# Kernel optimization log

Hardware: AMD Instinct MI355X
Metric: run time of the kernel (lower is better)

## Reference

```python
import jax, jax.numpy as jnp
import numpy as np

B, S, D, V = 4, 1024, 512, 8192
SCALES = [1, 2, 4, 8, 16]   # nn.Parameter init; used via int(scale.item()) -> static
WIN = 8                     # min(8, S//2) in compute_semantic_coherence
EPS = 1e-5


def layer_norm(x, g, b):
    m = x.mean(-1, keepdims=True)
    v = ((x - m) ** 2).mean(-1, keepdims=True)
    return (x - m) / jnp.sqrt(v + EPS) * g + b


def setup_inputs() -> dict:
    key = jax.random.key(0)
    ks = jax.random.split(key, 24)
    n = lambda k, shape, s=0.02: (jax.random.normal(k, shape, jnp.float32) * s)
    return {
        "embeddings": jax.random.normal(ks[0], (B, S, D), jnp.float32),
        "token_ids": jax.random.randint(ks[1], (B, S), 0, V),
        "context_mask": jnp.ones((B, S), jnp.float32),
        "token_similarity": n(ks[2], (V, V)),
        "W_scale": n(ks[3], (len(SCALES), D), 0.05), "b_scale": jnp.zeros((D,), jnp.float32),
        "W_sem": n(ks[4], (1, D), 0.05), "b_sem": jnp.zeros((D,), jnp.float32),
        "W_ctx": n(ks[5], (D, D), 0.02), "b_ctx": jnp.zeros((D,), jnp.float32),
        "W_fuse": n(ks[6], (4 * D, D), 0.02), "b_fuse": jnp.zeros((D,), jnp.float32),
        "ln1_g": jnp.ones((D,), jnp.float32), "ln1_b": jnp.zeros((D,), jnp.float32),
        "ln2_g": jnp.ones((D,), jnp.float32), "ln2_b": jnp.zeros((D,), jnp.float32),
        "ln3_g": jnp.ones((D,), jnp.float32), "ln3_b": jnp.zeros((D,), jnp.float32),
        "W_e0": n(ks[7], (D, D), 0.02), "b_e0": jnp.zeros((D,), jnp.float32),
        "W_e1": n(ks[8], (D, D), 0.02), "b_e1": jnp.zeros((D,), jnp.float32),
        "W_e2": n(ks[9], (D, D), 0.02), "b_e2": jnp.zeros((D,), jnp.float32),
    }


def _forward(embeddings, token_ids, context_mask, token_similarity,
             W_scale, b_scale, W_sem, b_sem, W_ctx, b_ctx, W_fuse, b_fuse,
             ln1_g, ln1_b, ln2_g, ln2_b, ln3_g, ln3_b,
             W_e0, b_e0, W_e1, b_e1, W_e2, b_e2):
    phases = jnp.tanh(embeddings)  # [B,S,D]

    # --- multi-scale coherence via cumulative sums + cos angle-difference identity ---
    # mean_t cos(p_t - m) = cos(m)*mean(cos p) + sin(m)*mean(sin p) over each window
    z = jnp.zeros((B, 1, D), phases.dtype)
    cum_p = jnp.concatenate([z, jnp.cumsum(phases, 1)], 1)            # [B,S+1,D]
    cum_c = jnp.concatenate([z, jnp.cumsum(jnp.cos(phases), 1)], 1)
    cum_s = jnp.concatenate([z, jnp.cumsum(jnp.sin(phases), 1)], 1)
    cols = []
    for s in SCALES:
        wm = (cum_p[:, s:] - cum_p[:, :-s]) / s   # window mean  [B,S-s+1,D]
        ac = (cum_c[:, s:] - cum_c[:, :-s]) / s   # window mean cos
        asn = (cum_s[:, s:] - cum_s[:, :-s]) / s  # window mean sin
        coh = jnp.mean(jnp.cos(wm) * ac + jnp.sin(wm) * asn, -1)      # [B,S-s+1]
        cols.append(jnp.pad(coh, ((0, 0), (0, s - 1))))               # torch leaves tail zeros
    msc = jnp.stack(cols, -1)                                         # [B,S,num_scales]
    scale_coh = msc @ W_scale + b_scale                               # [B,S,D]

    # --- semantic coherence (windowed, sim-weighted; torch takes mean over WHOLE tensor incl. batch) ---
    te = token_similarity[token_ids]                                  # [B,S,V]
    ten = te / jnp.maximum(jnp.linalg.norm(te, axis=-1, keepdims=True), 1e-12)
    tsim = jnp.einsum('biv,bjv->bij', ten, ten)                       # [B,S,S]
    off = jnp.arange(-WIN, WIN + 1)
    pos = jnp.arange(S)[:, None] + off[None, :]                       # [S,17]
    valid = (pos >= 0) & (pos < S)
    posc = jnp.clip(pos, 0, S - 1)
    pwin = phases[:, posc]                                            # [B,S,17,D]
    swin = jnp.take_along_axis(tsim, jnp.broadcast_to(posc[None], (B, S, 2 * WIN + 1)), axis=2)
    coh = jnp.cos((phases[:, :, None, :] - pwin) * swin[..., None]) * valid[None, :, :, None].astype(phases.dtype)
    counts = valid.sum(1).astype(phases.dtype)                        # [S]
    sem = coh.sum((0, 2, 3)) / (B * counts * D)                       # [S] (same scalar for all batches)
    sem = jnp.broadcast_to(sem[None, :], (B, S))[..., None]           # [B,S,1]
    sem_coh = sem @ W_sem + b_sem                                     # [B,S,D]

    # --- context coherence (context_mask path) ---
    cmean = jnp.mean(embeddings * context_mask[..., None], 1, keepdims=True)
    ctx_coh = jnp.cos(embeddings - cmean) @ W_ctx + b_ctx

    # --- local coherence ---
    lc = jnp.cos(embeddings[:, 1:] - embeddings[:, :-1])
    lc = jnp.concatenate([lc, jnp.zeros((B, 1, D), embeddings.dtype)], 1)

    allc = jnp.concatenate([scale_coh, sem_coh, ctx_coh, lc], -1)     # [B,S,4D]
    x = layer_norm(allc @ W_fuse + b_fuse, ln1_g, ln1_b)
    x = jax.nn.gelu(x, approximate=False)                             # dropout = identity (eval)
    for W, bb in ((W_e0, b_e0), (W_e1, b_e1), (W_e2, b_e2)):
        r = x
        h = layer_norm(x, ln2_g, ln2_b) @ W + bb
        x = r + jax.nn.gelu(h, approximate=False) * 0.1
    return layer_norm(x, ln3_g, ln3_b)


def reference(embeddings, token_ids, context_mask, token_similarity,
              W_scale, b_scale, W_sem, b_sem, W_ctx, b_ctx, W_fuse, b_fuse,
              ln1_g, ln1_b, ln2_g, ln2_b, ln3_g, ln3_b,
              W_e0, b_e0, W_e1, b_e1, W_e2, b_e2):
    return _forward(embeddings, token_ids, context_mask, token_similarity,
                    W_scale, b_scale, W_sem, b_sem, W_ctx, b_ctx, W_fuse, b_fuse,
                    ln1_g, ln1_b, ln2_g, ln2_b, ln3_g, ln3_b,
                    W_e0, b_e0, W_e1, b_e1, W_e2, b_e2)
```

## Files before the change

### kernel.cpp

```cpp
#include <hip/hip_runtime.h>


#define DEV __device__ __forceinline__
typedef unsigned short u16;
typedef __bf16 bf16x8 __attribute__((ext_vector_type(8)));
typedef float f32x4 __attribute__((ext_vector_type(4)));

static constexpr int S = 1024;
static constexpr int D = 512;
static constexpr int KCAT = 1056;

DEV u16 f2bf(float f) {
  unsigned u = __float_as_uint(f);
  return (u16)((u + 0x7fffu + ((u >> 16) & 1u)) >> 16);
}
DEV float gelu(float x) { return 0.5f * x * (1.f + erff(x * 0.70710678118654752f)); }
DEV float wred(float v) {
#pragma unroll
  for (int off = 32; off; off >>= 1) v += __shfl_down(v, off, 64);
  return v;
}
DEV void bred2(float& a, float& b, float* sm, int tid) {
  a = wred(a); b = wred(b);
  int w = tid >> 6;
  if ((tid & 63) == 0) { sm[w] = a; sm[w + 4] = b; }
  __syncthreads();
  a = sm[0] + sm[1] + sm[2] + sm[3];
  b = sm[4] + sm[5] + sm[6] + sm[7];
  __syncthreads();
}
DEV float qred(float v) {
  v += __shfl_xor(v, 1, 64);
  v += __shfl_xor(v, 2, 64);
  return v;
}

__global__ __launch_bounds__(256) void k_pre(const float* __restrict__ emb,
                                             const float* __restrict__ mask,
                                             float* __restrict__ ph,
                                             float* __restrict__ cmacc) {
  int blk = blockIdx.x, tid = threadIdx.x;
  if (blk < 1024) {
    int idx = blk * 256 + tid;
#pragma unroll
    for (int r = 0; r < 2; ++r, idx += 262144) {
      float4 v = ((const float4*)emb)[idx];
      float4 o;
      o.x = tanhf(v.x); o.y = tanhf(v.y); o.z = tanhf(v.z); o.w = tanhf(v.w);
      ((float4*)ph)[idx] = o;
    }
  } else {
    int r = blk - 1024, b = r >> 3, chunk = r & 7;
    float a0 = 0.f, a1 = 0.f;
    for (int s = chunk * 128; s < chunk * 128 + 128; ++s) {
      float m = mask[b * S + s];
      const float* row = emb + (size_t)(b * S + s) * D;
      a0 += row[tid] * m; a1 += row[tid + 256] * m;
    }
    atomicAdd(cmacc + b * D + tid, a0);
    atomicAdd(cmacc + b * D + tid + 256, a1);
  }
}

static constexpr int CP = 129;
__global__ __launch_bounds__(256) void k_dots(const float* __restrict__ sim,
                                              const int* __restrict__ tok,
                                              float* __restrict__ dots_raw,
                                              float* __restrict__ normsq) {
  __shared__ float sT[72 * CP];
  __shared__ int stok[72];
  int bx = blockIdx.x, cy = blockIdx.y, tid = threadIdx.x;
  int b = bx >> 4, g0 = (bx & 15) * 64, gidx = b * S + g0;
  if (tid < 72) {
    int p = g0 + tid;
    stok[tid] = (p < S) ? tok[b * S + p] : -1;
  }
  __syncthreads();
  const float4* sim4 = (const float4*)sim;
#pragma unroll
  for (int it = 0; it < 9; ++it) {
    int u = it * 256 + tid, r = u >> 5, q = u & 31;
    int tk = stok[r];
    float4 v = make_float4(0.f, 0.f, 0.f, 0.f);
    if (tk >= 0) v = sim4[(size_t)tk * 2048 + cy * 32 + q];
    float* dst = &sT[r * CP + 4 * q];
    dst[0] = v.x; dst[1] = v.y; dst[2] = v.z; dst[3] = v.w;
  }
  __syncthreads();
  int wave = tid >> 6, lane = tid & 63;
  float acc[9] = {};
  const float* base = &sT[lane * CP + wave * 32];
#pragma unroll 4
  for (int cc = 0; cc < 32; ++cc) {
    float va = base[cc];
    acc[8] += va * va;
#pragma unroll
    for (int o = 1; o <= 8; ++o) acc[o - 1] += va * base[o * CP + cc];
  }
  __syncthreads();
  float* red = sT;
#pragma unroll
  for (int s = 0; s < 9; ++s) red[(wave * 9 + s) * 64 + lane] = acc[s];
  __syncthreads();
  for (int u = tid; u < 576; u += 256) {
    int s = u >> 6, a = u & 63;
    float v = red[s * 64 + a] + red[(9 + s) * 64 + a] +
              red[(18 + s) * 64 + a] + red[(27 + s) * 64 + a];
    if (s < 8) atomicAdd(&dots_raw[(size_t)(gidx + a) * 8 + s], v);
    else       atomicAdd(&normsq[gidx + a], v);
  }
}

static constexpr int CP2 = 132;
__global__ __launch_bounds__(256) void k_coh(const float* __restrict__ ph,
                                             const float* __restrict__ dots_raw,
                                             const float* __restrict__ normsq,
                                             float* __restrict__ msc_raw,
                                             float* __restrict__ semacc) {
  __shared__ float sP[88 * CP2];
  __shared__ float sw2[64 * 17];
  int bx = blockIdx.x, dy = blockIdx.y, tid = threadIdx.x;
  int b = bx >> 4, g0 = (bx & 15) * 64;
  const float4* ph4 = (const float4*)ph;
#pragma unroll
  for (int it = 0; it < 11; ++it) {
    int u = it * 256 + tid, r = u >> 5, q = u & 31;
    int gr = g0 - 8 + r;
    gr = gr < 0 ? 0 : (gr > S - 1 ? S - 1 : gr);
    float4 v = ph4[(size_t)(b * S + gr) * 128 + dy * 32 + q];
    *(float4*)&sP[r * CP2 + 4 * q] = v;
  }
  for (int u = tid; u < 1088; u += 256) {
    int a = u / 17, oi = u - a * 17;
    int i = g0 + a, o = oi - 8, j = i + o;
    int idx = b * S + i;
    float v = 0.f;
    if (j >= 0 && j < S) {
      if (o == 0) v = 1.f;
      else {
        float dr = (o > 0) ? dots_raw[(size_t)idx * 8 + o - 1]
                           : dots_raw[(size_t)(idx + o) * 8 + (-o - 1)];
        float ni = fmaxf(sqrtf(normsq[idx]), 1e-12f);
        float nj = fmaxf(sqrtf(normsq[idx + o]), 1e-12f);
        v = dr / (ni * nj);
      }
    }
    sw2[u] = v;
  }
  __syncthreads();
  int ar = tid >> 2, dq = tid & 3;
  int i = g0 + ar, idx = b * S + i;
  int jmax = S - 1 - i; if (jmax > 15) jmax = 15;
  float swr[17];
#pragma unroll
  for (int oi = 0; oi < 17; ++oi) swr[oi] = sw2[ar * 17 + oi];
  float a0 = 0.f, a1 = 0.f, a2 = 0.f, a3 = 0.f, a4 = 0.f, asem = 0.f;
#pragma unroll 2
  for (int dd = 0; dd < 32; ++dd) {
    int d = dq + 4 * dd;
    const float* pb = &sP[(ar + 8) * CP2 + d];
    float sp = 0.f, sc = 0.f, ss = 0.f;
#pragma unroll
    for (int j = 0; j < 16; ++j) {
      float x = (j <= jmax) ? pb[j * CP2] : 0.f;
      sp += x; sc += __cosf(x); ss += __sinf(x);
      if (j == 0) a0 += __cosf(sp) * sc + __sinf(sp) * ss;
      else if (j == 1)  { float wm = sp * 0.5f;    a1 += __cosf(wm) * (sc * 0.5f)    + __sinf(wm) * (ss * 0.5f); }
      else if (j == 3)  { float wm = sp * 0.25f;   a2 += __cosf(wm) * (sc * 0.25f)   + __sinf(wm) * (ss * 0.25f); }
      else if (j == 7)  { float wm = sp * 0.125f;  a3 += __cosf(wm) * (sc * 0.125f)  + __sinf(wm) * (ss * 0.125f); }
      else if (j == 15) { float wm = sp * 0.0625f; a4 += __cosf(wm) * (sc * 0.0625f) + __sinf(wm) * (ss * 0.0625f); }
    }
    float p0 = pb[0];
    const float* qb = &sP[ar * CP2 + d];
#pragma unroll
    for (int oi = 0; oi < 17; ++oi) {
      int j = i + oi - 8;
      bool valid = (j >= 0) && (j < S);
      float pj = qb[oi * CP2];
      asem += valid ? __cosf((p0 - pj) * swr[oi]) : 0.f;
    }
  }
  a0 = qred(a0); a1 = qred(a1); a2 = qred(a2); a3 = qred(a3); a4 = qred(a4);
  asem = qred(asem);
  if (dq == 0) {
    float* mr = msc_raw + (size_t)idx * 5;
    atomicAdd(mr + 0, a0); atomicAdd(mr + 1, a1); atomicAdd(mr + 2, a2);
    atomicAdd(mr + 3, a3); atomicAdd(mr + 4, a4);
    atomicAdd(semacc + i, asem);
  }
}

__global__ __launch_bounds__(256) void k_wbig(const float* __restrict__ W0,
    const float* __restrict__ W1, const float* __restrict__ W2,
    const float* __restrict__ Wf, const float* __restrict__ wctx,
    const float* __restrict__ Wsc, const float* __restrict__ Wsm,
    const float* __restrict__ bsc, const float* __restrict__ bsm,
    const float* __restrict__ bcx,
    u16* __restrict__ T0, u16* __restrict__ T1, u16* __restrict__ T2,
    u16* __restrict__ wcatT, float* __restrict__ ctx_acc,
    float* __restrict__ sm_acc) {
  __shared__ float tile[64][65];
  int blk = blockIdx.x, tid = threadIdx.x;
  if (blk < 256) {
    int z = blk >> 6, rem = blk & 63;
    const float* src = z == 0 ? W0 : z == 1 ? W1 : z == 2 ? W2 : Wf + (size_t)1536 * 512;
    int r0 = (rem >> 3) * 64, c0 = (rem & 7) * 64;
    int tr = tid >> 6, tc = tid & 63;
#pragma unroll 4
    for (int i = 0; i < 16; ++i)
      tile[tr + i * 4][tc] = src[(size_t)(r0 + tr + i * 4) * 512 + c0 + tc];
    __syncthreads();
#pragma unroll 4
    for (int i = 0; i < 16; ++i) {
      int n = c0 + tr + i * 4, k = r0 + tc;
      u16 v = f2bf(tile[tc][tr + i * 4]);
      if (z == 3) wcatT[(size_t)n * KCAT + 512 + k] = v;
      else (z == 0 ? T0 : z == 1 ? T1 : T2)[(size_t)n * 512 + k] = v;
    }
  } else if (blk < 512) {
    int rem = blk - 256;
    int n = (rem & 1) * 256 + tid;
    int kbase = ((rem & 63) >> 1) * 16;
    int j0 = (rem >> 6) * 128;
    float acc[16] = {};
    for (int j = j0; j < j0 + 128; ++j) {
      float wf3 = Wf[(size_t)(1024 + j) * 512 + n];
#pragma unroll
      for (int kk = 0; kk < 16; ++kk) acc[kk] += wctx[(size_t)(kbase + kk) * 512 + j] * wf3;
    }
#pragma unroll
    for (int kk = 0; kk < 16; ++kk)
      atomicAdd(&ctx_acc[(size_t)(kbase + kk) * 512 + n], acc[kk]);
  } else {
    int rem = blk - 512;
    int n = (rem & 1) * 256 + tid;
    int j0 = (rem >> 1) * 16;
    float a0 = 0.f, a1 = 0.f, a2 = 0.f, a3 = 0.f, a4 = 0.f, au = 0.f, ac = 0.f;
    for (int j = j0; j < j0 + 16; ++j) {
      float wf1 = Wf[(size_t)j * 512 + n];
      float wf2 = Wf[(size_t)(512 + j) * 512 + n];
      float wf3 = Wf[(size_t)(1024 + j) * 512 + n];
      a0 += Wsc[j] * wf1; a1 += Wsc[512 + j] * wf1; a2 += Wsc[1024 + j] * wf1;
      a3 += Wsc[1536 + j] * wf1; a4 += Wsc[2048 + j] * wf1;
      au += Wsm[j] * wf2;
      ac += bsc[j] * wf1 + bsm[j] * wf2 + bcx[j] * wf3;
    }
    atomicAdd(&sm_acc[0 * 512 + n], a0);
    atomicAdd(&sm_acc[1 * 512 + n], a1);
    atomicAdd(&sm_acc[2 * 512 + n], a2);
    atomicAdd(&sm_acc[3 * 512 + n], a3);
    atomicAdd(&sm_acc[4 * 512 + n], a4);
    atomicAdd(&sm_acc[5 * 512 + n], au);
    atomicAdd(&sm_acc[6 * 512 + n], ac);
  }
}

__global__ __launch_bounds__(256) void k_packfin(const float* __restrict__ ctx_acc,
    const float* __restrict__ sm_acc, const float* __restrict__ bfu,
    u16* __restrict__ wcatT) {
  __shared__ float tile[64][65];
  int blk = blockIdx.x, tid = threadIdx.x;
  if (blk < 64) {
    int r0 = (blk >> 3) * 64, c0 = (blk & 7) * 64;
    int tr = tid >> 6, tc = tid & 63;
#pragma unroll 4
    for (int i = 0; i < 16; ++i)
      tile[tr + i * 4][tc] = ctx_acc[(size_t)(r0 + tr + i * 4) * 512 + c0 + tc];
    __syncthreads();
#pragma unroll 4
    for (int i = 0; i < 16; ++i)
      wcatT[(size_t)(c0 + tr + i * 4) * KCAT + r0 + tc] = f2bf(tile[tc][tr + i * 4]);
  } else {
    int n = (blk - 64) * 256 + tid;
    u16* row = wcatT + (size_t)n * KCAT;
#pragma unroll
    for (int s = 0; s < 6; ++s) row[1024 + s] = f2bf(sm_acc[s * 512 + n]);
    row[1030] = f2bf(sm_acc[6 * 512 + n] + bfu[n]);
    for (int k = 1031; k < KCAT; ++k) row[k] = 0;
  }
}

__global__ __launch_bounds__(256) void k_xcat(const float* __restrict__ emb,
    const float* __restrict__ cmacc, const float* __restrict__ msc_raw,
    const float* __restrict__ semacc, u16* __restrict__ xcat) {
  int idx = blockIdx.x, b = idx >> 10, i = idx & 1023, tid = threadIdx.x;
  const float* erow = emb + (size_t)idx * D;
  u16* orow = xcat + (size_t)idx * KCAT;
  for (int c = tid; c < KCAT; c += 256) {
    float v;
    if (c < 512) {
      v = __cosf(erow[c] - cmacc[b * D + c] * (1.f / 1024.f));
    } else if (c < 1024) {
      int d = c - 512;
      v = (i < S - 1) ? __cosf(erow[D + d] - erow[d]) : 0.f;
    } else if (c < 1029) {
      int s = c - 1024, req = (1 << s) - 1;
      v = (S - 1 - i >= req) ? msc_raw[(size_t)idx * 5 + s] * (1.f / 512.f) : 0.f;
    } else if (c == 1029) {
      int cnt = ((i < 8) ? i : 8) + ((S - 1 - i < 8) ? (S - 1 - i) : 8) + 1;
      v = semacc[i] / (4.f * (float)cnt * 512.f);
    } else if (c == 1030) {
      v = 1.f;
    } else v = 0.f;
    orow[c] = f2bf(v);
  }
}

__global__ __launch_bounds__(256) void k_gemm(const u16* __restrict__ A,
    const u16* __restrict__ BT, float* __restrict__ C,
    const float* __restrict__ bias, int K) {
  __shared__ __align__(16) u16 sA[64 * 40];
  __shared__ __align__(16) u16 sB[64 * 40];
  int tid = threadIdx.x, wave = tid >> 6, lane = tid & 63;
  int m0 = blockIdx.x * 64, n0 = blockIdx.y * 64;
  int lr = tid >> 2, lc = (tid & 3) * 8;
  int q8 = (lane >> 4) * 8, l15 = lane & 15;
  const u16* Ap = A + (size_t)(m0 + lr) * K + lc;
  const u16* Bp = BT + (size_t)(n0 + lr) * K + lc;
  f32x4 acc[4] = {};
  for (int k0 = 0; k0 < K; k0 += 32) {
    *(uint4*)&sA[lr * 40 + lc] = *(const uint4*)(Ap + k0);
    *(uint4*)&sB[lr * 40 + lc] = *(const uint4*)(Bp + k0);
    __syncthreads();
    bf16x8 af = *(const bf16x8*)&sA[(wave * 16 + l15) * 40 + q8];
#pragma unroll
    for (int f = 0; f < 4; ++f) {
      bf16x8 bfr = *(const bf16x8*)&sB[(f * 16 + l15) * 40 + q8];
      acc[f] = __builtin_amdgcn_mfma_f32_16x16x32_bf16(af, bfr, acc[f], 0, 0, 0);
    }
    __syncthreads();
  }
  int r0 = m0 + wave * 16 + (lane >> 4) * 4;
#pragma unroll
  for (int f = 0; f < 4; ++f) {
    int col = n0 + f * 16 + l15;
    float bv = bias ? bias[col] : 0.f;
#pragma unroll
    for (int r = 0; r < 4; ++r)
      C[(size_t)(r0 + r) * 512 + col] = acc[f][r] + bv;
  }
}

__global__ __launch_bounds__(256) void k_post_y1(const float* __restrict__ y,
    float* __restrict__ x, u16* __restrict__ t,
    const float* __restrict__ g1, const float* __restrict__ b1,
    const float* __restrict__ g2, const float* __restrict__ b2) {
  __shared__ float sm[8];
  int row = blockIdx.x, tid = threadIdx.x;
  size_t base = (size_t)row * 512;
  float v0 = y[base + tid], v1 = y[base + tid + 256];
  float s = v0 + v1, ss = v0 * v0 + v1 * v1;
  bred2(s, ss, sm, tid);
  float m = s * (1.f / 512.f);
  float inv = rsqrtf(ss * (1.f / 512.f) - m * m + 1e-5f);
  float x0 = gelu((v0 - m) * inv * g1[tid] + b1[tid]);
  float x1 = gelu((v1 - m) * inv * g1[tid + 256] + b1[tid + 256]);
  x[base + tid] = x0; x[base + tid + 256] = x1;
  s = x0 + x1; ss = x0 * x0 + x1 * x1;
  bred2(s, ss, sm, tid);
  m = s * (1.f / 512.f);
  inv = rsqrtf(ss * (1.f / 512.f) - m * m + 1e-5f);
  t[base + tid] = f2bf((x0 - m) * inv * g2[tid] + b2[tid]);
  t[base + tid + 256] = f2bf((x1 - m) * inv * g2[tid + 256] + b2[tid + 256]);
}

__global__ __launch_bounds__(256) void k_post_res(const float* __restrict__ h,
    float* __restrict__ x, u16* __restrict__ t, float* __restrict__ out,
    const float* __restrict__ g, const float* __restrict__ bb, int final_) {
  __shared__ float sm[8];
  int row = blockIdx.x, tid = threadIdx.x;
  size_t base = (size_t)row * 512;
  float x0 = x[base + tid] + 0.1f * gelu(h[base + tid]);
  float x1 = x[base + tid + 256] + 0.1f * gelu(h[base + tid + 256]);
  float s = x0 + x1, ss = x0 * x0 + x1 * x1;
  bred2(s, ss, sm, tid);
  float m = s * (1.f / 512.f);
  float inv = rsqrtf(ss * (1.f / 512.f) - m * m + 1e-5f);
  float n0 = (x0 - m) * inv * g[tid] + bb[tid];
  float n1 = (x1 - m) * inv * g[tid + 256] + bb[tid + 256];
  if (final_) {
    out[base + tid] = n0; out[base + tid + 256] = n1;
  } else {
    x[base + tid] = x0; x[base + tid + 256] = x1;
    t[base + tid] = f2bf(n0); t[base + tid + 256] = f2bf(n1);
  }
}

extern "C" void kernel_launch(void* const* d_in, const int* in_sizes, int n_in,
                              void* d_out, int out_size, void* d_ws, size_t ws_size,
                              hipStream_t stream) {
  const float* emb     = (const float*)d_in[0];
  const int*   tok     = (const int*)d_in[1];
  const float* mask    = (const float*)d_in[2];
  const float* sim     = (const float*)d_in[3];
  const float* W_scale = (const float*)d_in[4];
  const float* b_scale = (const float*)d_in[5];
  const float* W_sem   = (const float*)d_in[6];
  const float* b_sem   = (const float*)d_in[7];
  const float* W_ctx   = (const float*)d_in[8];
  const float* b_ctx   = (const float*)d_in[9];
  const float* W_fuse  = (const float*)d_in[10];
  const float* b_fuse  = (const float*)d_in[11];
  const float* ln1_g = (const float*)d_in[12], *ln1_b = (const float*)d_in[13];
  const float* ln2_g = (const float*)d_in[14], *ln2_b = (const float*)d_in[15];
  const float* ln3_g = (const float*)d_in[16], *ln3_b = (const float*)d_in[17];
  const float* W_e0 = (const float*)d_in[18], *b_e0 = (const float*)d_in[19];
  const float* W_e1 = (const float*)d_in[20], *b_e1 = (const float*)d_in[21];
  const float* W_e2 = (const float*)d_in[22], *b_e2 = (const float*)d_in[23];
  float* out = (float*)d_out;

  char* w = (char*)d_ws; size_t off = 0;
  auto alloc = [&](size_t bytes) { void* p = w + off; off += (bytes + 255) & ~(size_t)255; return p; };
  float* phases = (float*)alloc((size_t)4096 * 512 * 4);
  float* hbuf   = (float*)alloc((size_t)4096 * 512 * 4);
  float* xbuf   = (float*)alloc((size_t)4096 * 512 * 4);
  u16*   tbuf   = (u16*)  alloc((size_t)4096 * 512 * 2);
  u16*   xcat   = (u16*)  alloc((size_t)4096 * KCAT * 2);
  u16*   wcatT  = (u16*)  alloc((size_t)512 * KCAT * 2);
  u16*   We0T   = (u16*)  alloc((size_t)512 * 512 * 2);
  u16*   We1T   = (u16*)  alloc((size_t)512 * 512 * 2);
  u16*   We2T   = (u16*)  alloc((size_t)512 * 512 * 2);
  float* semacc   = (float*)alloc((size_t)1024 * 4);
  float* cmacc    = (float*)alloc((size_t)4 * 512 * 4);
  float* dots_raw = (float*)alloc((size_t)4096 * 8 * 4);
  float* normsq   = (float*)alloc((size_t)4096 * 4);
  float* msc_raw  = (float*)alloc((size_t)4096 * 5 * 4);
  float* ctx_acc  = (float*)alloc((size_t)512 * 512 * 4);
  float* sm_acc   = (float*)alloc((size_t)7 * 512 * 4);
  (void)ws_size; (void)in_sizes; (void)n_in; (void)out_size;

  size_t zbytes = (size_t)(1024 + 4 * 512 + 4096 * 8 + 4096 + 4096 * 5 + 512 * 512 + 7 * 512) * 4;
  hipMemsetAsync(semacc, 0, zbytes, stream);

  k_pre<<<1056, 256, 0, stream>>>(emb, mask, phases, cmacc);
  k_dots<<<dim3(64, 64), 256, 0, stream>>>(sim, tok, dots_raw, normsq);
  k_coh<<<dim3(64, 4), 256, 0, stream>>>(phases, dots_raw, normsq, msc_raw, semacc);

  k_wbig<<<576, 256, 0, stream>>>(W_e0, W_e1, W_e2, W_fuse, W_ctx,
                                  W_scale, W_sem, b_scale, b_sem, b_ctx,
                                  We0T, We1T, We2T, wcatT, ctx_acc, sm_acc);
  k_packfin<<<66, 256, 0, stream>>>(ctx_acc, sm_acc, b_fuse, wcatT);

  k_xcat<<<4096, 256, 0, stream>>>(emb, cmacc, msc_raw, semacc, xcat);
  k_gemm<<<dim3(64, 8), 256, 0, stream>>>(xcat, wcatT, hbuf, nullptr, KCAT);
  k_post_y1<<<4096, 256, 0, stream>>>(hbuf, xbuf, tbuf, ln1_g, ln1_b, ln2_g, ln2_b);

  k_gemm<<<dim3(64, 8), 256, 0, stream>>>(tbuf, We0T, hbuf, b_e0, 512);
  k_post_res<<<4096, 256, 0, stream>>>(hbuf, xbuf, tbuf, nullptr, ln2_g, ln2_b, 0);
  k_gemm<<<dim3(64, 8), 256, 0, stream>>>(tbuf, We1T, hbuf, b_e1, 512);
  k_post_res<<<4096, 256, 0, stream>>>(hbuf, xbuf, tbuf, nullptr, ln2_g, ln2_b, 0);
  k_gemm<<<dim3(64, 8), 256, 0, stream>>>(tbuf, We2T, hbuf, b_e2, 512);
  k_post_res<<<4096, 256, 0, stream>>>(hbuf, xbuf, nullptr, out, ln3_g, ln3_b, 1);
}
```

Before: 609.6 us.

## Fuse residual MLP stack into one kernel, fold tanh and pre-kernels into neighbors

Replaces the three GEMM plus post-LN launches of the residual stack with a single k_resnet kernel. Each 32-row block keeps x in registers, applies LayerNorm into LDS, and runs the bf16 MFMA GEMMs with bias and GELU in the epilogue. The k_pre kernel goes away: tanh is computed on the fly in k_coh and the masked context sum moves into k_wbig, while k_packfin merges into k_xcat. This cuts launch count and intermediate HBM round-trips, but k_resnet launches only 128 blocks that read weights straight from global memory, which may leave the GPU underused.

```diff
diff --git a/kernel.cpp b/kernel.cpp
--- a/kernel.cpp
+++ b/kernel.cpp
@@ -33,33 +33,6 @@
   v += __shfl_xor(v, 1, 64);
   v += __shfl_xor(v, 2, 64);
   return v;
-}
-
-__global__ __launch_bounds__(256) void k_pre(const float* __restrict__ emb,
-                                             const float* __restrict__ mask,
-                                             float* __restrict__ ph,
-                                             float* __restrict__ cmacc) {
-  int blk = blockIdx.x, tid = threadIdx.x;
-  if (blk < 1024) {
-    int idx = blk * 256 + tid;
-#pragma unroll
-    for (int r = 0; r < 2; ++r, idx += 262144) {
-      float4 v = ((const float4*)emb)[idx];
-      float4 o;
-      o.x = tanhf(v.x); o.y = tanhf(v.y); o.z = tanhf(v.z); o.w = tanhf(v.w);
-      ((float4*)ph)[idx] = o;
-    }
-  } else {
-    int r = blk - 1024, b = r >> 3, chunk = r & 7;
-    float a0 = 0.f, a1 = 0.f;
-    for (int s = chunk * 128; s < chunk * 128 + 128; ++s) {
-      float m = mask[b * S + s];
-      const float* row = emb + (size_t)(b * S + s) * D;
-      a0 += row[tid] * m; a1 += row[tid + 256] * m;
-    }
-    atomicAdd(cmacc + b * D + tid, a0);
-    atomicAdd(cmacc + b * D + tid + 256, a1);
-  }
 }
 
 static constexpr int CP = 129;
@@ -112,7 +85,7 @@
 }
 
 static constexpr int CP2 = 132;
-__global__ __launch_bounds__(256) void k_coh(const float* __restrict__ ph,
+__global__ __launch_bounds__(256) void k_coh(const float* __restrict__ emb,
                                              const float* __restrict__ dots_raw,
                                              const float* __restrict__ normsq,
                                              float* __restrict__ msc_raw,
@@ -121,13 +94,14 @@
   __shared__ float sw2[64 * 17];
   int bx = blockIdx.x, dy = blockIdx.y, tid = threadIdx.x;
   int b = bx >> 4, g0 = (bx & 15) * 64;
-  const float4* ph4 = (const float4*)ph;
+  const float4* emb4 = (const float4*)emb;
 #pragma unroll
   for (int it = 0; it < 11; ++it) {
     int u = it * 256 + tid, r = u >> 5, q = u & 31;
     int gr = g0 - 8 + r;
     gr = gr < 0 ? 0 : (gr > S - 1 ? S - 1 : gr);
-    float4 v = ph4[(size_t)(b * S + gr) * 128 + dy * 32 + q];
+    float4 v = emb4[(size_t)(b * S + gr) * 128 + dy * 32 + q];
+    v.x = tanhf(v.x); v.y = tanhf(v.y); v.z = tanhf(v.z); v.w = tanhf(v.w);
     *(float4*)&sP[r * CP2 + 4 * q] = v;
   }
   for (int u = tid; u < 1088; u += 256) {
@@ -195,10 +169,11 @@
     const float* __restrict__ Wf, const float* __restrict__ wctx,
     const float* __restrict__ Wsc, const float* __restrict__ Wsm,
     const float* __restrict__ bsc, const float* __restrict__ bsm,
-    const float* __restrict__ bcx,
+    const float* __restrict__ bcx, const float* __restrict__ emb,
+    const float* __restrict__ mask,
     u16* __restrict__ T0, u16* __restrict__ T1, u16* __restrict__ T2,
     u16* __restrict__ wcatT, float* __restrict__ ctx_acc,
-    float* __restrict__ sm_acc) {
+    float* __restrict__ sm_acc, float* __restrict__ cmacc) {
   __shared__ float tile[64][65];
   int blk = blockIdx.x, tid = threadIdx.x;
   if (blk < 256) {
@@ -231,7 +206,7 @@
 #pragma unroll
     for (int kk = 0; kk < 16; ++kk)
       atomicAdd(&ctx_acc[(size_t)(kbase + kk) * 512 + n], acc[kk]);
-  } else {
+  } else if (blk < 576) {
     int rem = blk - 512;
     int n = (rem & 1) * 256 + tid;
     int j0 = (rem >> 1) * 16;
@@ -252,16 +227,51 @@
     atomicAdd(&sm_acc[4 * 512 + n], a4);
     atomicAdd(&sm_acc[5 * 512 + n], au);
     atomicAdd(&sm_acc[6 * 512 + n], ac);
-  }
-}
-
-__global__ __launch_bounds__(256) void k_packfin(const float* __restrict__ ctx_acc,
+  } else {
+    int r = blk - 576, b = r >> 3, chunk = r & 7;
+    float a0 = 0.f, a1 = 0.f;
+    for (int s = chunk * 128; s < chunk * 128 + 128; ++s) {
+      float m = mask[b * S + s];
+      const float* row = emb + (size_t)(b * S + s) * D;
+      a0 += row[tid] * m; a1 += row[tid + 256] * m;
+    }
+    atomicAdd(cmacc + b * D + tid, a0);
+    atomicAdd(cmacc + b * D + tid + 256, a1);
+  }
+}
+
+__global__ __launch_bounds__(256) void k_xcat(const float* __restrict__ emb,
+    const float* __restrict__ cmacc, const float* __restrict__ msc_raw,
+    const float* __restrict__ semacc, const float* __restrict__ ctx_acc,
     const float* __restrict__ sm_acc, const float* __restrict__ bfu,
-    u16* __restrict__ wcatT) {
+    u16* __restrict__ xcat, u16* __restrict__ wcatT) {
   __shared__ float tile[64][65];
   int blk = blockIdx.x, tid = threadIdx.x;
-  if (blk < 64) {
-    int r0 = (blk >> 3) * 64, c0 = (blk & 7) * 64;
+  if (blk < 4096) {
+    int idx = blk, b = idx >> 10, i = idx & 1023;
+    const float* erow = emb + (size_t)idx * D;
+    u16* orow = xcat + (size_t)idx * KCAT;
+    for (int c = tid; c < KCAT; c += 256) {
+      float v;
+      if (c < 512) {
+        v = __cosf(erow[c] - cmacc[b * D + c] * (1.f / 1024.f));
+      } else if (c < 1024) {
+        int d = c - 512;
+        v = (i < S - 1) ? __cosf(erow[D + d] - erow[d]) : 0.f;
+      } else if (c < 1029) {
+        int s = c - 1024, req = (1 << s) - 1;
+        v = (S - 1 - i >= req) ? msc_raw[(size_t)idx * 5 + s] * (1.f / 512.f) : 0.f;
+      } else if (c == 1029) {
+        int cnt = ((i < 8) ? i : 8) + ((S - 1 - i < 8) ? (S - 1 - i) : 8) + 1;
+        v = semacc[i] / (4.f * (float)cnt * 512.f);
+      } else if (c == 1030) {
+        v = 1.f;
+      } else v = 0.f;
+      orow[c] = f2bf(v);
+    }
+  } else if (blk < 4160) {
+    int rem = blk - 4096;
+    int r0 = (rem >> 3) * 64, c0 = (rem & 7) * 64;
     int tr = tid >> 6, tc = tid & 63;
 #pragma unroll 4
     for (int i = 0; i < 16; ++i)
@@ -271,7 +281,7 @@
     for (int i = 0; i < 16; ++i)
       wcatT[(size_t)(c0 + tr + i * 4) * KCAT + r0 + tc] = f2bf(tile[tc][tr + i * 4]);
   } else {
-    int n = (blk - 64) * 256 + tid;
+    int n = (blk - 4160) * 256 + tid;
     u16* row = wcatT + (size_t)n * KCAT;
 #pragma unroll
     for (int s = 0; s < 6; ++s) row[1024 + s] = f2bf(sm_acc[s * 512 + n]);
@@ -280,35 +290,8 @@
   }
 }
 
-__global__ __launch_bounds__(256) void k_xcat(const float* __restrict__ emb,
-    const float* __restrict__ cmacc, const float* __restrict__ msc_raw,
-    const float* __restrict__ semacc, u16* __restrict__ xcat) {
-  int idx = blockIdx.x, b = idx >> 10, i = idx & 1023, tid = threadIdx.x;
-  const float* erow = emb + (size_t)idx * D;
-  u16* orow = xcat + (size_t)idx * KCAT;
-  for (int c = tid; c < KCAT; c += 256) {
-    float v;
-    if (c < 512) {
-      v = __cosf(erow[c] - cmacc[b * D + c] * (1.f / 1024.f));
-    } else if (c < 1024) {
-      int d = c - 512;
-      v = (i < S - 1) ? __cosf(erow[D + d] - erow[d]) : 0.f;
-    } else if (c < 1029) {
-      int s = c - 1024, req = (1 << s) - 1;
-      v = (S - 1 - i >= req) ? msc_raw[(size_t)idx * 5 + s] * (1.f / 512.f) : 0.f;
-    } else if (c == 1029) {
-      int cnt = ((i < 8) ? i : 8) + ((S - 1 - i < 8) ? (S - 1 - i) : 8) + 1;
-      v = semacc[i] / (4.f * (float)cnt * 512.f);
-    } else if (c == 1030) {
-      v = 1.f;
-    } else v = 0.f;
-    orow[c] = f2bf(v);
-  }
-}
-
 __global__ __launch_bounds__(256) void k_gemm(const u16* __restrict__ A,
-    const u16* __restrict__ BT, float* __restrict__ C,
-    const float* __restrict__ bias, int K) {
+    const u16* __restrict__ BT, float* __restrict__ C, int K) {
   __shared__ __align__(16) u16 sA[64 * 40];
   __shared__ __align__(16) u16 sB[64 * 40];
   int tid = threadIdx.x, wave = tid >> 6, lane = tid & 63;
@@ -334,17 +317,14 @@
 #pragma unroll
   for (int f = 0; f < 4; ++f) {
     int col = n0 + f * 16 + l15;
-    float bv = bias ? bias[col] : 0.f;
 #pragma unroll
     for (int r = 0; r < 4; ++r)
-      C[(size_t)(r0 + r) * 512 + col] = acc[f][r] + bv;
+      C[(size_t)(r0 + r) * 512 + col] = acc[f][r];
   }
 }
 
 __global__ __launch_bounds__(256) void k_post_y1(const float* __restrict__ y,
-    float* __restrict__ x, u16* __restrict__ t,
-    const float* __restrict__ g1, const float* __restrict__ b1,
-    const float* __restrict__ g2, const float* __restrict__ b2) {
+    float* __restrict__ x, const float* __restrict__ g1, const float* __restrict__ b1) {
   __shared__ float sm[8];
   int row = blockIdx.x, tid = threadIdx.x;
   size_t base = (size_t)row * 512;
@@ -353,36 +333,120 @@
   bred2(s, ss, sm, tid);
   float m = s * (1.f / 512.f);
   float inv = rsqrtf(ss * (1.f / 512.f) - m * m + 1e-5f);
-  float x0 = gelu((v0 - m) * inv * g1[tid] + b1[tid]);
-  float x1 = gelu((v1 - m) * inv * g1[tid + 256] + b1[tid + 256]);
-  x[base + tid] = x0; x[base + tid + 256] = x1;
-  s = x0 + x1; ss = x0 * x0 + x1 * x1;
-  bred2(s, ss, sm, tid);
-  m = s * (1.f / 512.f);
-  inv = rsqrtf(ss * (1.f / 512.f) - m * m + 1e-5f);
-  t[base + tid] = f2bf((x0 - m) * inv * g2[tid] + b2[tid]);
-  t[base + tid + 256] = f2bf((x1 - m) * inv * g2[tid + 256] + b2[tid + 256]);
-}
-
-__global__ __launch_bounds__(256) void k_post_res(const float* __restrict__ h,
-    float* __restrict__ x, u16* __restrict__ t, float* __restrict__ out,
-    const float* __restrict__ g, const float* __restrict__ bb, int final_) {
-  __shared__ float sm[8];
-  int row = blockIdx.x, tid = threadIdx.x;
-  size_t base = (size_t)row * 512;
-  float x0 = x[base + tid] + 0.1f * gelu(h[base + tid]);
-  float x1 = x[base + tid + 256] + 0.1f * gelu(h[base + tid + 256]);
-  float s = x0 + x1, ss = x0 * x0 + x1 * x1;
-  bred2(s, ss, sm, tid);
-  float m = s * (1.f / 512.f);
-  float inv = rsqrtf(ss * (1.f / 512.f) - m * m + 1e-5f);
-  float n0 = (x0 - m) * inv * g[tid] + bb[tid];
-  float n1 = (x1 - m) * inv * g[tid + 256] + bb[tid + 256];
-  if (final_) {
-    out[base + tid] = n0; out[base + tid + 256] = n1;
-  } else {
-    x[base + tid] = x0; x[base + tid + 256] = x1;
-    t[base + tid] = f2bf(n0); t[base + tid + 256] = f2bf(n1);
+  x[base + tid] = gelu((v0 - m) * inv * g1[tid] + b1[tid]);
+  x[base + tid + 256] = gelu((v1 - m) * inv * g1[tid + 256] + b1[tid + 256]);
+}
+
+__global__ __launch_bounds__(256) void k_resnet(const float* __restrict__ xin,
+    const u16* __restrict__ W0, const u16* __restrict__ W1, const u16* __restrict__ W2,
+    const float* __restrict__ be0, const float* __restrict__ be1, const float* __restrict__ be2,
+    const float* __restrict__ g2, const float* __restrict__ b2v,
+    const float* __restrict__ g3, const float* __restrict__ b3v,
+    float* __restrict__ out) {
+  __shared__ u16 tl[32 * 520];
+  __shared__ float rsm[4][32][2];
+  int tid = threadIdx.x, wave = tid >> 6, lane = tid & 63;
+  int q = lane >> 4, l15 = lane & 15, q8 = q * 8;
+  int r0 = blockIdx.x * 32, ncol = wave * 128;
+  float xr[2][8][4];
+  float g2c[8], b2c[8];
+#pragma unroll
+  for (int f = 0; f < 8; ++f) {
+    int col = ncol + f * 16 + l15;
+    g2c[f] = g2[col]; b2c[f] = b2v[col];
+#pragma unroll
+    for (int mf = 0; mf < 2; ++mf)
+#pragma unroll
+      for (int r = 0; r < 4; ++r)
+        xr[mf][f][r] = xin[(size_t)(r0 + mf * 16 + q * 4 + r) * 512 + col];
+  }
+  const u16* Wt[3] = {W0, W1, W2};
+  const float* bet[3] = {be0, be1, be2};
+#pragma unroll 1
+  for (int L = 0; L < 4; ++L) {
+    float s[2][4], ss[2][4];
+#pragma unroll
+    for (int mf = 0; mf < 2; ++mf)
+#pragma unroll
+      for (int r = 0; r < 4; ++r) {
+        float a = 0.f, b = 0.f;
+#pragma unroll
+        for (int f = 0; f < 8; ++f) { float v = xr[mf][f][r]; a += v; b += v * v; }
+#pragma unroll
+        for (int m = 8; m; m >>= 1) { a += __shfl_xor(a, m, 64); b += __shfl_xor(b, m, 64); }
+        s[mf][r] = a; ss[mf][r] = b;
+      }
+    if (l15 == 0) {
+#pragma unroll
+      for (int mf = 0; mf < 2; ++mf)
+#pragma unroll
+        for (int r = 0; r < 4; ++r) {
+          rsm[wave][mf * 16 + q * 4 + r][0] = s[mf][r];
+          rsm[wave][mf * 16 + q * 4 + r][1] = ss[mf][r];
+        }
+    }
+    __syncthreads();
+    float mean[2][4], inv[2][4];
+#pragma unroll
+    for (int mf = 0; mf < 2; ++mf)
+#pragma unroll
+      for (int r = 0; r < 4; ++r) {
+        int row = mf * 16 + q * 4 + r;
+        float su = rsm[0][row][0] + rsm[1][row][0] + rsm[2][row][0] + rsm[3][row][0];
+        float sq = rsm[0][row][1] + rsm[1][row][1] + rsm[2][row][1] + rsm[3][row][1];
+        float m = su * (1.f / 512.f);
+        mean[mf][r] = m;
+        inv[mf][r] = rsqrtf(sq * (1.f / 512.f) - m * m + 1e-5f);
+      }
+    if (L == 3) {
+#pragma unroll
+      for (int mf = 0; mf < 2; ++mf)
+#pragma unroll
+        for (int f = 0; f < 8; ++f) {
+          int col = ncol + f * 16 + l15;
+          float gg = g3[col], bb = b3v[col];
+#pragma unroll
+          for (int r = 0; r < 4; ++r)
+            out[(size_t)(r0 + mf * 16 + q * 4 + r) * 512 + col] =
+                (xr[mf][f][r] - mean[mf][r]) * inv[mf][r] * gg + bb;
+        }
+      return;
+    }
+#pragma unroll
+    for (int mf = 0; mf < 2; ++mf)
+#pragma unroll
+      for (int f = 0; f < 8; ++f) {
+        int col = ncol + f * 16 + l15;
+#pragma unroll
+        for (int r = 0; r < 4; ++r)
+          tl[(mf * 16 + q * 4 + r) * 520 + col] =
+              f2bf((xr[mf][f][r] - mean[mf][r]) * inv[mf][r] * g2c[f] + b2c[f]);
+      }
+    __syncthreads();
+    const u16* W = Wt[L];
+    f32x4 acc[2][8] = {};
+    for (int k0 = 0; k0 < 512; k0 += 32) {
+      bf16x8 af0 = *(const bf16x8*)&tl[l15 * 520 + k0 + q8];
+      bf16x8 af1 = *(const bf16x8*)&tl[(16 + l15) * 520 + k0 + q8];
+#pragma unroll
+      for (int f = 0; f < 8; ++f) {
+        bf16x8 bfr = *(const bf16x8*)(W + (size_t)(ncol + f * 16 + l15) * 512 + k0 + q8);
+        acc[0][f] = __builtin_amdgcn_mfma_f32_16x16x32_bf16(af0, bfr, acc[0][f], 0, 0, 0);
+        acc[1][f] = __builtin_amdgcn_mfma_f32_16x16x32_bf16(af1, bfr, acc[1][f], 0, 0, 0);
+      }
+    }
+    __syncthreads();
+    const float* be = bet[L];
+#pragma unroll
+    for (int f = 0; f < 8; ++f) {
+      int col = ncol + f * 16 + l15;
+      float bv = be[col];
+#pragma unroll
+      for (int mf = 0; mf < 2; ++mf)
+#pragma unroll
+        for (int r = 0; r < 4; ++r)
+          xr[mf][f][r] += 0.1f * gelu(acc[mf][f][r] + bv);
+    }
   }
 }
 
@@ -411,10 +475,8 @@
 
   char* w = (char*)d_ws; size_t off = 0;
   auto alloc = [&](size_t bytes) { void* p = w + off; off += (bytes + 255) & ~(size_t)255; return p; };
-  float* phases = (float*)alloc((size_t)4096 * 512 * 4);
   float* hbuf   = (float*)alloc((size_t)4096 * 512 * 4);
   float* xbuf   = (float*)alloc((size_t)4096 * 512 * 4);
-  u16*   tbuf   = (u16*)  alloc((size_t)4096 * 512 * 2);
   u16*   xcat   = (u16*)  alloc((size_t)4096 * KCAT * 2);
   u16*   wcatT  = (u16*)  alloc((size_t)512 * KCAT * 2);
   u16*   We0T   = (u16*)  alloc((size_t)512 * 512 * 2);
@@ -432,23 +494,15 @@
   size_t zbytes = (size_t)(1024 + 4 * 512 + 4096 * 8 + 4096 + 4096 * 5 + 512 * 512 + 7 * 512) * 4;
   hipMemsetAsync(semacc, 0, zbytes, stream);
 
-  k_pre<<<1056, 256, 0, stream>>>(emb, mask, phases, cmacc);
   k_dots<<<dim3(64, 64), 256, 0, stream>>>(sim, tok, dots_raw, normsq);
-  k_coh<<<dim3(64, 4), 256, 0, stream>>>(phases, dots_raw, normsq, msc_raw, semacc);
-
-  k_wbig<<<576, 256, 0, stream>>>(W_e0, W_e1, W_e2, W_fuse, W_ctx,
-                                  W_scale, W_sem, b_scale, b_sem, b_ctx,
-                                  We0T, We1T, We2T, wcatT, ctx_acc, sm_acc);
-  k_packfin<<<66, 256, 0, stream>>>(ctx_acc, sm_acc, b_fuse, wcatT);
-
-  k_xcat<<<4096, 256, 0, stream>>>(emb, cmacc, msc_raw, semacc, xcat);
-  k_gemm<<<dim3(64, 8), 256, 0, stream>>>(xcat, wcatT, hbuf, nullptr, KCAT);
-  k_post_y1<<<4096, 256, 0, stream>>>(hbuf, xbuf, tbuf, ln1_g, ln1_b, ln2_g, ln2_b);
-
-  k_gemm<<<dim3(64, 8), 256, 0, stream>>>(tbuf, We0T, hbuf, b_e0, 512);
-  k_post_res<<<4096, 256, 0, stream>>>(hbuf, xbuf, tbuf, nullptr, ln2_g, ln2_b, 0);
-  k_gemm<<<dim3(64, 8), 256, 0, stream>>>(tbuf, We1T, hbuf, b_e1, 512);
-  k_post_res<<<4096, 256, 0, stream>>>(hbuf, xbuf, tbuf, nullptr, ln2_g, ln2_b, 0);
-  k_gemm<<<dim3(64, 8), 256, 0, stream>>>(tbuf, We2T, hbuf, b_e2, 512);
-  k_post_res<<<4096, 256, 0, stream>>>(hbuf, xbuf, nullptr, out, ln3_g, ln3_b, 1);
-}
+  k_wbig<<<608, 256, 0, stream>>>(W_e0, W_e1, W_e2, W_fuse, W_ctx,
+                                  W_scale, W_sem, b_scale, b_sem, b_ctx, emb, mask,
+                                  We0T, We1T, We2T, wcatT, ctx_acc, sm_acc, cmacc);
+  k_coh<<<dim3(64, 4), 256, 0, stream>>>(emb, dots_raw, normsq, msc_raw, semacc);
+  k_xcat<<<4162, 256, 0, stream>>>(emb, cmacc, msc_raw, semacc, ctx_acc, sm_acc,
+                                   b_fuse, xcat, wcatT);
+  k_gemm<<<dim3(64, 8), 256, 0, stream>>>(xcat, wcatT, hbuf, KCAT);
+  k_post_y1<<<4096, 256, 0, stream>>>(hbuf, xbuf, ln1_g, ln1_b);
+  k_resnet<<<128, 256, 0, stream>>>(xbuf, We0T, We1T, We2T, b_e0, b_e1, b_e2,
+                                    ln2_g, ln2_b, ln3_g, ln3_b, out);
+}
```

After: 615.3 us. About the same (+0.9%).
